# Kernel optimization log

Measured on AMD Instinct MI355X. Metric: run time of the kernel, lower is better.

Reference implementation:

```python
import jax, jax.numpy as jnp
import numpy as np

N_HEADS = 16
HEAD_DIM = 64
HIDDEN = 1024
LN_EPS = 1e-6

def setup_inputs() -> dict:
    key = jax.random.key(0)
    ks = jax.random.split(key, 8)
    B, L, H = 2, 2048, HIDDEN
    s = 1.0 / np.sqrt(H)
    return {
        "q": jax.random.normal(ks[0], (B, L, H), jnp.float32),
        "k": jax.random.normal(ks[1], (B, L, H), jnp.float32),
        "v": jax.random.normal(ks[2], (B, L, H), jnp.float32),
        "w_qs": jax.random.normal(ks[3], (H, N_HEADS * HEAD_DIM), jnp.float32) * s,
        "w_ks": jax.random.normal(ks[4], (H, N_HEADS * HEAD_DIM), jnp.float32) * s,
        "w_vs": jax.random.normal(ks[5], (H, N_HEADS * HEAD_DIM), jnp.float32) * s,
        "w_fc": jax.random.normal(ks[6], (N_HEADS * HEAD_DIM, H), jnp.float32) * s,
        "ln_gamma": jnp.ones((H,), jnp.float32),
        "ln_beta": jnp.zeros((H,), jnp.float32),
    }

def reference(q, k, v, w_qs, w_ks, w_vs, w_fc, ln_gamma, ln_beta):
    B, Lq, H = q.shape
    residual = q
    # projections -> [B, heads, L, head_dim]
    qh = (q @ w_qs).reshape(B, Lq, N_HEADS, HEAD_DIM).transpose(0, 2, 1, 3)
    kh = (k @ w_ks).reshape(B, -1, N_HEADS, HEAD_DIM).transpose(0, 2, 1, 3)
    vh = (v @ w_vs).reshape(B, -1, N_HEADS, HEAD_DIM).transpose(0, 2, 1, 3)
    temp = jnp.asarray(HEAD_DIM ** 0.5, qh.dtype)
    scores = jnp.einsum("bhqd,bhkd->bhqk", qh / temp, kh)  # [B,H,Lq,Lk]
    attn = jax.nn.softmax(scores, axis=-1)  # dropout = identity (eval)
    out = jnp.einsum("bhqk,bhkd->bhqd", attn, vh)
    out = out.transpose(0, 2, 1, 3).reshape(B, Lq, N_HEADS * HEAD_DIM)
    out = out @ w_fc  # dropout = identity (eval)
    x = residual + out
    mu = jnp.mean(x, axis=-1, keepdims=True)
    var = jnp.var(x, axis=-1, keepdims=True)
    y = (x - mu) * jax.lax.rsqrt(var + LN_EPS) * ln_gamma + ln_beta
    return (y, attn)
```

## Files before the change

kernel.cpp:

```cpp
#include <hip/hip_runtime.h>
#include <stdint.h>

#define NHEADS 16
#define HDIM   64
#define HID    1024
#define SEQ    2048
#define NB     2

typedef short s16x8 __attribute__((ext_vector_type(8)));
typedef float f32x4 __attribute__((ext_vector_type(4)));

__device__ __forceinline__ short f2bf(float f) {
  union { float f; unsigned u; } x; x.f = f;
  unsigned r = (x.u + 0x7FFFu + ((x.u >> 16) & 1u)) >> 16;
  return (short)r;
}

__device__ __forceinline__ void gload16(const void* g, void* l) {
  __builtin_amdgcn_global_load_lds(
      (const __attribute__((address_space(1))) unsigned int*)g,
      (__attribute__((address_space(3))) unsigned int*)l, 16, 0, 0);
}

__global__ __launch_bounds__(256)
void prep(const float* __restrict__ w0, const float* __restrict__ w1,
          const float* __restrict__ w2, const float* __restrict__ w3,
          const float* __restrict__ q, const float* __restrict__ k,
          const float* __restrict__ v,
          unsigned short* __restrict__ d0, unsigned short* __restrict__ d1,
          unsigned short* __restrict__ d2, unsigned short* __restrict__ d3,
          unsigned short* __restrict__ qb, unsigned short* __restrict__ kb,
          unsigned short* __restrict__ vb)
{
  const int z = blockIdx.z;
  if (z < 4) {
    const float* src = z == 0 ? w0 : z == 1 ? w1 : z == 2 ? w2 : w3;
    unsigned short* dst = z == 0 ? d0 : z == 1 ? d1 : z == 2 ? d2 : d3;
    __shared__ float t[32][33];
    const int tx = threadIdx.x & 31, ty = threadIdx.x >> 5;
    const int x0 = (blockIdx.x & 31) * 32, y0 = (blockIdx.x >> 5) * 32;
#pragma unroll
    for (int i = 0; i < 4; ++i) {
      const int r = ty + i * 8;
      t[r][tx] = src[(size_t)(y0 + r) * HID + (x0 + tx)];
    }
    __syncthreads();
#pragma unroll
    for (int i = 0; i < 4; ++i) {
      const int r = ty + i * 8;
      dst[(size_t)(x0 + r) * HID + (y0 + tx)] = (unsigned short)f2bf(t[tx][r]);
    }
  } else {
    const float* s = z == 4 ? q : z == 5 ? k : v;
    unsigned short* d = z == 4 ? qb : z == 5 ? kb : vb;
#pragma unroll
    for (int c = 0; c < 2; ++c) {
      const size_t i = (size_t)blockIdx.x * 4096 + c * 2048 + threadIdx.x * 8;
      const float4 f0 = ((const float4*)(s + i))[0];
      const float4 f1 = ((const float4*)(s + i))[1];
      s16x8 o;
      o[0] = f2bf(f0.x); o[1] = f2bf(f0.y); o[2] = f2bf(f0.z); o[3] = f2bf(f0.w);
      o[4] = f2bf(f1.x); o[5] = f2bf(f1.y); o[6] = f2bf(f1.z); o[7] = f2bf(f1.w);
      *(s16x8*)(d + i) = o;
    }
  }
}

__global__ __launch_bounds__(256, 3)
void proj_gemm(const unsigned short* __restrict__ qb, const unsigned short* __restrict__ kb,
               const unsigned short* __restrict__ vb,
               const unsigned short* __restrict__ wqt, const unsigned short* __restrict__ wkt,
               const unsigned short* __restrict__ wvt,
               unsigned short* __restrict__ Qh, unsigned short* __restrict__ Kh,
               unsigned short* __restrict__ Vt)
{
  __shared__ unsigned short As[128 * 64];
  __shared__ unsigned short Bs[128 * 64];
  const int tid = threadIdx.x, lane = tid & 63, w = tid >> 6;
  const int lg = lane >> 4, ll = lane & 15;
  const int wm = w & 1, wn = w >> 1;
  const int z = blockIdx.z;
  const int m0 = blockIdx.x * 128, n0 = blockIdx.y * 128;
  const int xorv = (ll & 7) << 4;

  const unsigned short* A  = z == 0 ? qb : z == 1 ? kb : vb;
  const unsigned short* Bt = z == 0 ? wqt : z == 1 ? wkt : wvt;
  const float alpha = z == 0 ? 0.125f : 1.0f;

  f32x4 acc[4][4];
#pragma unroll
  for (int m = 0; m < 4; ++m)
#pragma unroll
    for (int n = 0; n < 4; ++n) acc[m][n] = (f32x4)0.f;

  int rS[4], cbS[4];
#pragma unroll
  for (int c = 0; c < 4; ++c) {
    const int b = (w * 4 + c) * 1024 + lane * 16;
    rS[c] = b >> 7;
    cbS[c] = (b & 127) ^ ((rS[c] & 7) << 4);
  }

  for (int k0 = 0; k0 < HID; k0 += 64) {
    __syncthreads();
#pragma unroll
    for (int c = 0; c < 4; ++c) {
      gload16((const char*)A + ((((size_t)(m0 + rS[c]) * HID + k0) << 1) + cbS[c]),
              (char*)As + (w * 4 + c) * 1024);
      gload16((const char*)Bt + ((((size_t)(n0 + rS[c]) * HID + k0) << 1) + cbS[c]),
              (char*)Bs + (w * 4 + c) * 1024);
    }
    __syncthreads();
#pragma unroll
    for (int kk = 0; kk < 2; ++kk) {
      const int cb2 = kk * 64 + lg * 16;
      s16x8 a[4], b[4];
#pragma unroll
      for (int m = 0; m < 4; ++m)
        a[m] = *(const s16x8*)((const char*)As + ((((wm * 64 + m * 16 + ll) << 7) + cb2) ^ xorv));
#pragma unroll
      for (int n = 0; n < 4; ++n)
        b[n] = *(const s16x8*)((const char*)Bs + ((((wn * 64 + n * 16 + ll) << 7) + cb2) ^ xorv));
#pragma unroll
      for (int m = 0; m < 4; ++m)
#pragma unroll
        for (int n = 0; n < 4; ++n)
          acc[m][n] = __builtin_amdgcn_mfma_f32_16x16x32_bf16(a[m], b[n], acc[m][n], 0, 0, 0);
    }
  }

#pragma unroll
  for (int m = 0; m < 4; ++m)
#pragma unroll
    for (int n = 0; n < 4; ++n)
#pragma unroll
      for (int r = 0; r < 4; ++r) {
        const int row = m0 + wm * 64 + m * 16 + lg * 4 + r;
        const int col = n0 + wn * 64 + n * 16 + ll;
        const int bb = row >> 11, l = row & (SEQ - 1);
        const int h = col >> 6, d = col & (HDIM - 1);
        const unsigned short o = (unsigned short)f2bf(acc[m][n][r] * alpha);
        if (z < 2) {
          unsigned short* out = z == 0 ? Qh : Kh;
          out[(((size_t)(bb * NHEADS + h) * SEQ + l) * HDIM) + d] = o;
        } else {
          Vt[(((size_t)(bb * NHEADS + h) * HDIM + d) * SEQ) + l] = o;
        }
      }
}

__global__ __launch_bounds__(256, 4)
void fc_gemm(const unsigned short* __restrict__ A, const unsigned short* __restrict__ Bt,
             float* __restrict__ C, const float* __restrict__ resid)
{
  __shared__ unsigned short As[64 * 64];
  __shared__ unsigned short Bs[128 * 64];
  const int tid = threadIdx.x, lane = tid & 63, w = tid >> 6;
  const int lg = lane >> 4, ll = lane & 15;
  const int wm = w & 1, wn = w >> 1;
  const int m0 = blockIdx.x * 64, n0 = blockIdx.y * 128;
  const int xorv = (ll & 7) << 4;

  f32x4 acc[2][4];
#pragma unroll
  for (int m = 0; m < 2; ++m)
#pragma unroll
    for (int n = 0; n < 4; ++n) acc[m][n] = (f32x4)0.f;

  int rA[2], cA[2], rB[4], cB[4];
#pragma unroll
  for (int c = 0; c < 2; ++c) {
    const int b = (w * 2 + c) * 1024 + lane * 16;
    rA[c] = b >> 7; cA[c] = (b & 127) ^ ((rA[c] & 7) << 4);
  }
#pragma unroll
  for (int c = 0; c < 4; ++c) {
    const int b = (w * 4 + c) * 1024 + lane * 16;
    rB[c] = b >> 7; cB[c] = (b & 127) ^ ((rB[c] & 7) << 4);
  }

  for (int k0 = 0; k0 < HID; k0 += 64) {
    __syncthreads();
#pragma unroll
    for (int c = 0; c < 2; ++c)
      gload16((const char*)A + ((((size_t)(m0 + rA[c]) * HID + k0) << 1) + cA[c]),
              (char*)As + (w * 2 + c) * 1024);
#pragma unroll
    for (int c = 0; c < 4; ++c)
      gload16((const char*)Bt + ((((size_t)(n0 + rB[c]) * HID + k0) << 1) + cB[c]),
              (char*)Bs + (w * 4 + c) * 1024);
    __syncthreads();
#pragma unroll
    for (int kk = 0; kk < 2; ++kk) {
      const int cb2 = kk * 64 + lg * 16;
      s16x8 a[2], b[4];
#pragma unroll
      for (int m = 0; m < 2; ++m)
        a[m] = *(const s16x8*)((const char*)As + ((((wm * 32 + m * 16 + ll) << 7) + cb2) ^ xorv));
#pragma unroll
      for (int n = 0; n < 4; ++n)
        b[n] = *(const s16x8*)((const char*)Bs + ((((wn * 64 + n * 16 + ll) << 7) + cb2) ^ xorv));
#pragma unroll
      for (int m = 0; m < 2; ++m)
#pragma unroll
        for (int n = 0; n < 4; ++n)
          acc[m][n] = __builtin_amdgcn_mfma_f32_16x16x32_bf16(a[m], b[n], acc[m][n], 0, 0, 0);
    }
  }

#pragma unroll
  for (int m = 0; m < 2; ++m)
#pragma unroll
    for (int n = 0; n < 4; ++n)
#pragma unroll
      for (int r = 0; r < 4; ++r) {
        const int row = m0 + wm * 32 + m * 16 + lg * 4 + r;
        const int col = n0 + wn * 64 + n * 16 + ll;
        const size_t idx = (size_t)row * HID + col;
        C[idx] = acc[m][n][r] + resid[idx];
      }
}

__global__ __launch_bounds__(256, 3)
void fused_attn(const unsigned short* __restrict__ Qh,
                const unsigned short* __restrict__ Kh,
                const unsigned short* __restrict__ Vt,
                float* __restrict__ attn,
                unsigned short* __restrict__ Ofc)
{
  __shared__ unsigned short BufA[128 * 64];
  __shared__ unsigned short BufB[128 * 64];
  __shared__ unsigned short Ps[128][72];
  const int tid = threadIdx.x, lane = tid & 63, w = tid >> 6;
  const int lg = lane >> 4, ll = lane & 15;
  const int xorv = (ll & 7) << 4;

  const int lin = blockIdx.y * gridDim.x + blockIdx.x;
  const int lin2 = (lin & 7) * 64 + (lin >> 3);
  const int z = lin2 >> 4, qb = lin2 & 15;
  const int bb = z >> 4, h = z & 15;
  const int m0 = qb * 128;

  const unsigned short* Qz = Qh + (size_t)z * SEQ * HDIM;
  const unsigned short* Kz = Kh + (size_t)z * SEQ * HDIM;
  const unsigned short* Vz = Vt + (size_t)z * HDIM * SEQ;
  float* Az = attn + (size_t)z * SEQ * SEQ;

  int rK[4], cbK[4], rV[4], cbV[4];
#pragma unroll
  for (int c = 0; c < 4; ++c) {
    const int b = (w * 4 + c) * 1024 + lane * 16;
    rK[c] = b >> 7; cbK[c] = (b & 127) ^ ((rK[c] & 7) << 4);
    rV[c] = b >> 8; cbV[c] = (b & 255) ^ ((rV[c] & 7) << 4);
  }

  s16x8 qf[2][2];
#pragma unroll
  for (int m = 0; m < 2; ++m)
#pragma unroll
    for (int kk = 0; kk < 2; ++kk)
      qf[m][kk] = *(const s16x8*)(Qz + (size_t)(m0 + w * 32 + m * 16 + ll) * HDIM
                                  + kk * 32 + lg * 8);

  float sml[8];
#pragma unroll
  for (int i = 0; i < 8; ++i) sml[i] = 0.f;

#pragma unroll
  for (int c = 0; c < 4; ++c)
    gload16((const char*)Kz + ((((size_t)(0 * 128 + rK[c]) * HDIM) << 1) + cbK[c]),
            (char*)BufA + (w * 4 + c) * 1024);
  __syncthreads();
  for (int j = 0; j < 16; ++j) {
    char* cur = (char*)((j & 1) ? BufB : BufA);
    char* nxt = (char*)((j & 1) ? BufA : BufB);
    if (j < 15) {
#pragma unroll
      for (int c = 0; c < 4; ++c)
        gload16((const char*)Kz + ((((size_t)((j + 1) * 128 + rK[c]) * HDIM) << 1) + cbK[c]),
                nxt + (w * 4 + c) * 1024);
    }
    f32x4 s[2][8];
#pragma unroll
    for (int m = 0; m < 2; ++m)
#pragma unroll
      for (int n = 0; n < 8; ++n) s[m][n] = (f32x4)0.f;
#pragma unroll
    for (int kk = 0; kk < 2; ++kk) {
      const int cb2 = kk * 64 + lg * 16;
      s16x8 bk[8];
#pragma unroll
      for (int n = 0; n < 8; ++n)
        bk[n] = *(const s16x8*)(cur + ((((n * 16 + ll) << 7) + cb2) ^ xorv));
#pragma unroll
      for (int m = 0; m < 2; ++m)
#pragma unroll
        for (int n = 0; n < 8; ++n)
          s[m][n] = __builtin_amdgcn_mfma_f32_16x16x32_bf16(qf[m][kk], bk[n], s[m][n], 0, 0, 0);
    }
#pragma unroll
    for (int m = 0; m < 2; ++m)
#pragma unroll
      for (int r = 0; r < 4; ++r) {
        const int i = m * 4 + r;
#pragma unroll
        for (int n = 0; n < 8; ++n) sml[i] += __expf(s[m][n][r]);
      }
    __syncthreads();
  }
  float inv[8];
#pragma unroll
  for (int i = 0; i < 8; ++i) {
    float su = sml[i];
#pragma unroll
    for (int off = 1; off < 16; off <<= 1) su += __shfl_xor(su, off, 64);
    inv[i] = 1.0f / su;
  }

  f32x4 ao[2][4];
#pragma unroll
  for (int m = 0; m < 2; ++m)
#pragma unroll
    for (int n = 0; n < 4; ++n) ao[m][n] = (f32x4)0.f;

  for (int j = 0; j < 16; ++j) {
    __syncthreads();
#pragma unroll
    for (int c = 0; c < 4; ++c) {
      gload16((const char*)Kz + ((((size_t)(j * 128 + rK[c]) * HDIM) << 1) + cbK[c]),
              (char*)BufA + (w * 4 + c) * 1024);
      gload16((const char*)Vz + ((((size_t)rV[c] * SEQ + j * 128) << 1) + cbV[c]),
              (char*)BufB + (w * 4 + c) * 1024);
    }
    __syncthreads();
    f32x4 s[2][8];
#pragma unroll
    for (int m = 0; m < 2; ++m)
#pragma unroll
      for (int n = 0; n < 8; ++n) s[m][n] = (f32x4)0.f;
#pragma unroll
    for (int kk = 0; kk < 2; ++kk) {
      const int cb2 = kk * 64 + lg * 16;
      s16x8 bk[8];
#pragma unroll
      for (int n = 0; n < 8; ++n)
        bk[n] = *(const s16x8*)((const char*)BufA + ((((n * 16 + ll) << 7) + cb2) ^ xorv));
#pragma unroll
      for (int m = 0; m < 2; ++m)
#pragma unroll
        for (int n = 0; n < 8; ++n)
          s[m][n] = __builtin_amdgcn_mfma_f32_16x16x32_bf16(qf[m][kk], bk[n], s[m][n], 0, 0, 0);
    }
#pragma unroll
    for (int h2 = 0; h2 < 2; ++h2) {
#pragma unroll
      for (int m = 0; m < 2; ++m)
#pragma unroll
        for (int r = 0; r < 4; ++r) {
          const int i = m * 4 + r;
          const int rowl = w * 32 + m * 16 + lg * 4 + r;
          float* dst = Az + (size_t)(m0 + rowl) * SEQ + j * 128 + h2 * 64 + ll;
#pragma unroll
          for (int nn = 0; nn < 4; ++nn) {
            const float p = __expf(s[m][h2 * 4 + nn][r]) * inv[i];
            __builtin_nontemporal_store(p, dst + nn * 16);
            Ps[rowl][nn * 16 + ll] = (unsigned short)f2bf(p);
          }
        }
#pragma unroll
      for (int kkl = 0; kkl < 2; ++kkl) {
        const int cb2v = (h2 * 2 + kkl) * 64 + lg * 16;
        s16x8 pa[2], vbf[4];
#pragma unroll
        for (int m = 0; m < 2; ++m)
          pa[m] = *(const s16x8*)&Ps[w * 32 + m * 16 + ll][kkl * 32 + lg * 8];
#pragma unroll
        for (int n = 0; n < 4; ++n)
          vbf[n] = *(const s16x8*)((const char*)BufB + ((((n * 16 + ll) << 8) + cb2v) ^ xorv));
#pragma unroll
        for (int m = 0; m < 2; ++m)
#pragma unroll
          for (int n = 0; n < 4; ++n)
            ao[m][n] = __builtin_amdgcn_mfma_f32_16x16x32_bf16(pa[m], vbf[n], ao[m][n], 0, 0, 0);
      }
    }
  }

#pragma unroll
  for (int m = 0; m < 2; ++m)
#pragma unroll
    for (int n = 0; n < 4; ++n)
#pragma unroll
      for (int r = 0; r < 4; ++r) {
        const int qrow = m0 + w * 32 + m * 16 + lg * 4 + r;
        const int d = n * 16 + ll;
        Ofc[((size_t)bb * SEQ + qrow) * HID + h * HDIM + d] =
            (unsigned short)f2bf(ao[m][n][r]);
      }
}

__global__ __launch_bounds__(256)
void ln_kernel(const float* __restrict__ x, const float* __restrict__ gamma,
               const float* __restrict__ beta, float* __restrict__ y)
{
  const int tid = threadIdx.x;
  const size_t row = blockIdx.x;
  const float4 v = ((const float4*)(x + row * HID))[tid];
  float s = v.x + v.y + v.z + v.w;
  float q = v.x * v.x + v.y * v.y + v.z * v.z + v.w * v.w;
#pragma unroll
  for (int off = 32; off; off >>= 1) {
    s += __shfl_xor(s, off, 64);
    q += __shfl_xor(q, off, 64);
  }
  __shared__ float ps[4], pq[4];
  const int wid = tid >> 6, lane = tid & 63;
  if (lane == 0) { ps[wid] = s; pq[wid] = q; }
  __syncthreads();
  const float ts = ps[0] + ps[1] + ps[2] + ps[3];
  const float tq = pq[0] + pq[1] + pq[2] + pq[3];
  const float mu = ts * (1.0f / HID);
  const float var = tq * (1.0f / HID) - mu * mu;
  const float rs = rsqrtf(var + 1e-6f);
  const float4 g = ((const float4*)gamma)[tid];
  const float4 bb = ((const float4*)beta)[tid];
  float4 o;
  o.x = (v.x - mu) * rs * g.x + bb.x;
  o.y = (v.y - mu) * rs * g.y + bb.y;
  o.z = (v.z - mu) * rs * g.z + bb.z;
  o.w = (v.w - mu) * rs * g.w + bb.w;
  ((float4*)(y + row * HID))[tid] = o;
}

extern "C" void kernel_launch(void* const* d_in, const int* in_sizes, int n_in,
                              void* d_out, int out_size, void* d_ws, size_t ws_size,
                              hipStream_t stream)
{
  (void)in_sizes; (void)n_in; (void)out_size; (void)ws_size;
  const float* q     = (const float*)d_in[0];
  const float* k     = (const float*)d_in[1];
  const float* v     = (const float*)d_in[2];
  const float* w_qs  = (const float*)d_in[3];
  const float* w_ks  = (const float*)d_in[4];
  const float* w_vs  = (const float*)d_in[5];
  const float* w_fc  = (const float*)d_in[6];
  const float* gamma = (const float*)d_in[7];
  const float* beta  = (const float*)d_in[8];

  char* ws = (char*)d_ws;
  unsigned short* wqt = (unsigned short*)(ws);
  unsigned short* wkt = (unsigned short*)(ws + ((size_t)2 << 20));
  unsigned short* wvt = (unsigned short*)(ws + ((size_t)4 << 20));
  unsigned short* wft = (unsigned short*)(ws + ((size_t)6 << 20));
  unsigned short* qb  = (unsigned short*)(ws + ((size_t)8 << 20));
  unsigned short* kb  = (unsigned short*)(ws + ((size_t)16 << 20));
  unsigned short* vb  = (unsigned short*)(ws + ((size_t)24 << 20));
  unsigned short* Qh  = (unsigned short*)(ws + ((size_t)32 << 20));
  unsigned short* Kh  = (unsigned short*)(ws + ((size_t)40 << 20));
  unsigned short* Vt  = (unsigned short*)(ws + ((size_t)48 << 20));
  unsigned short* Ofc = qb;
  float*          xres = (float*)(ws + ((size_t)16 << 20));

  float* y_out = (float*)d_out;
  float* attn  = (float*)d_out + (size_t)NB * SEQ * HID;

  const dim3 b256(256, 1, 1);

  prep<<<dim3(1024, 1, 7), b256, 0, stream>>>(
      w_qs, w_ks, w_vs, w_fc, q, k, v, wqt, wkt, wvt, wft, qb, kb, vb);

  proj_gemm<<<dim3(32, 8, 3), b256, 0, stream>>>(qb, kb, vb, wqt, wkt, wvt, Qh, Kh, Vt);

  fused_attn<<<dim3(16, 32, 1), b256, 0, stream>>>(Qh, Kh, Vt, attn, Ofc);

  fc_gemm<<<dim3(64, 8, 1), b256, 0, stream>>>(Ofc, wft, xres, q);

  ln_kernel<<<dim3(NB * SEQ, 1, 1), b256, 0, stream>>>(xres, gamma, beta, y_out);
}
```

Baseline: 246.5 us.

## Double-buffer K/V loads in attention second pass with 64-key tiles

The second attention pass previously loaded a 128-key K tile and V tile into shared memory synchronously each iteration, with two barriers. It now uses 64-key tiles, double-buffered, prefetching the next K/V tiles with async global-to-LDS loads while computing the current one, and keeps one barrier per iteration. Shared memory is merged into one base array so the buffers can be split differently across the two passes. The cost is twice as many iterations and barriers, plus a smaller per-iteration work granule.

```diff
diff --git a/kernel.cpp b/kernel.cpp
--- a/kernel.cpp
+++ b/kernel.cpp
@@ -228,9 +228,8 @@
                 float* __restrict__ attn,
                 unsigned short* __restrict__ Ofc)
 {
-  __shared__ unsigned short BufA[128 * 64];
-  __shared__ unsigned short BufB[128 * 64];
-  __shared__ unsigned short Ps[128][72];
+  __shared__ char sbase[32 * 1024 + 128 * 72 * 2];
+  unsigned short (*Ps)[72] = (unsigned short (*)[72])(sbase + 32 * 1024);
   const int tid = threadIdx.x, lane = tid & 63, w = tid >> 6;
   const int lg = lane >> 4, ll = lane & 15;
   const int xorv = (ll & 7) << 4;
@@ -246,12 +245,17 @@
   const unsigned short* Vz = Vt + (size_t)z * HDIM * SEQ;
   float* Az = attn + (size_t)z * SEQ * SEQ;
 
-  int rK[4], cbK[4], rV[4], cbV[4];
+  int rK[4], cbK[4];
 #pragma unroll
   for (int c = 0; c < 4; ++c) {
     const int b = (w * 4 + c) * 1024 + lane * 16;
     rK[c] = b >> 7; cbK[c] = (b & 127) ^ ((rK[c] & 7) << 4);
-    rV[c] = b >> 8; cbV[c] = (b & 255) ^ ((rV[c] & 7) << 4);
+  }
+  int r2[2], cb2s[2];
+#pragma unroll
+  for (int c = 0; c < 2; ++c) {
+    const int b = (w * 2 + c) * 1024 + lane * 16;
+    r2[c] = b >> 7; cb2s[c] = (b & 127) ^ ((r2[c] & 7) << 4);
   }
 
   s16x8 qf[2][2];
@@ -268,12 +272,12 @@
 
 #pragma unroll
   for (int c = 0; c < 4; ++c)
-    gload16((const char*)Kz + ((((size_t)(0 * 128 + rK[c]) * HDIM) << 1) + cbK[c]),
-            (char*)BufA + (w * 4 + c) * 1024);
+    gload16((const char*)Kz + ((((size_t)rK[c] * HDIM) << 1) + cbK[c]),
+            sbase + (w * 4 + c) * 1024);
   __syncthreads();
   for (int j = 0; j < 16; ++j) {
-    char* cur = (char*)((j & 1) ? BufB : BufA);
-    char* nxt = (char*)((j & 1) ? BufA : BufB);
+    char* cur = sbase + (j & 1) * 16384;
+    char* nxt = sbase + ((j & 1) ^ 1) * 16384;
     if (j < 15) {
 #pragma unroll
       for (int c = 0; c < 4; ++c)
@@ -323,67 +327,77 @@
 #pragma unroll
     for (int n = 0; n < 4; ++n) ao[m][n] = (f32x4)0.f;
 
-  for (int j = 0; j < 16; ++j) {
-    __syncthreads();
-#pragma unroll
-    for (int c = 0; c < 4; ++c) {
-      gload16((const char*)Kz + ((((size_t)(j * 128 + rK[c]) * HDIM) << 1) + cbK[c]),
-              (char*)BufA + (w * 4 + c) * 1024);
-      gload16((const char*)Vz + ((((size_t)rV[c] * SEQ + j * 128) << 1) + cbV[c]),
-              (char*)BufB + (w * 4 + c) * 1024);
-    }
-    __syncthreads();
-    f32x4 s[2][8];
+#pragma unroll
+  for (int c = 0; c < 2; ++c) {
+    gload16((const char*)Kz + ((((size_t)r2[c] * HDIM) << 1) + cb2s[c]),
+            sbase + (w * 2 + c) * 1024);
+    gload16((const char*)Vz + ((((size_t)r2[c] * SEQ) << 1) + cb2s[c]),
+            sbase + 16384 + (w * 2 + c) * 1024);
+  }
+  __syncthreads();
+  for (int j = 0; j < 32; ++j) {
+    char* curK = sbase + (j & 1) * 8192;
+    char* curV = sbase + 16384 + (j & 1) * 8192;
+    char* nxtK = sbase + ((j & 1) ^ 1) * 8192;
+    char* nxtV = sbase + 16384 + ((j & 1) ^ 1) * 8192;
+    if (j < 31) {
+#pragma unroll
+      for (int c = 0; c < 2; ++c) {
+        gload16((const char*)Kz + ((((size_t)((j + 1) * 64 + r2[c]) * HDIM) << 1) + cb2s[c]),
+                nxtK + (w * 2 + c) * 1024);
+        gload16((const char*)Vz + ((((size_t)(r2[c] * SEQ + (j + 1) * 64)) << 1) + cb2s[c]),
+                nxtV + (w * 2 + c) * 1024);
+      }
+    }
+    f32x4 s[2][4];
 #pragma unroll
     for (int m = 0; m < 2; ++m)
 #pragma unroll
-      for (int n = 0; n < 8; ++n) s[m][n] = (f32x4)0.f;
+      for (int n = 0; n < 4; ++n) s[m][n] = (f32x4)0.f;
 #pragma unroll
     for (int kk = 0; kk < 2; ++kk) {
       const int cb2 = kk * 64 + lg * 16;
-      s16x8 bk[8];
-#pragma unroll
-      for (int n = 0; n < 8; ++n)
-        bk[n] = *(const s16x8*)((const char*)BufA + ((((n * 16 + ll) << 7) + cb2) ^ xorv));
-#pragma unroll
-      for (int m = 0; m < 2; ++m)
-#pragma unroll
-        for (int n = 0; n < 8; ++n)
+      s16x8 bk[4];
+#pragma unroll
+      for (int n = 0; n < 4; ++n)
+        bk[n] = *(const s16x8*)(curK + ((((n * 16 + ll) << 7) + cb2) ^ xorv));
+#pragma unroll
+      for (int m = 0; m < 2; ++m)
+#pragma unroll
+        for (int n = 0; n < 4; ++n)
           s[m][n] = __builtin_amdgcn_mfma_f32_16x16x32_bf16(qf[m][kk], bk[n], s[m][n], 0, 0, 0);
     }
 #pragma unroll
-    for (int h2 = 0; h2 < 2; ++h2) {
-#pragma unroll
-      for (int m = 0; m < 2; ++m)
-#pragma unroll
-        for (int r = 0; r < 4; ++r) {
-          const int i = m * 4 + r;
-          const int rowl = w * 32 + m * 16 + lg * 4 + r;
-          float* dst = Az + (size_t)(m0 + rowl) * SEQ + j * 128 + h2 * 64 + ll;
-#pragma unroll
-          for (int nn = 0; nn < 4; ++nn) {
-            const float p = __expf(s[m][h2 * 4 + nn][r]) * inv[i];
-            __builtin_nontemporal_store(p, dst + nn * 16);
-            Ps[rowl][nn * 16 + ll] = (unsigned short)f2bf(p);
-          }
+    for (int m = 0; m < 2; ++m)
+#pragma unroll
+      for (int r = 0; r < 4; ++r) {
+        const int i = m * 4 + r;
+        const int rowl = w * 32 + m * 16 + lg * 4 + r;
+        float* dst = Az + (size_t)(m0 + rowl) * SEQ + j * 64 + ll;
+#pragma unroll
+        for (int nn = 0; nn < 4; ++nn) {
+          const float p = __expf(s[m][nn][r]) * inv[i];
+          __builtin_nontemporal_store(p, dst + nn * 16);
+          Ps[rowl][nn * 16 + ll] = (unsigned short)f2bf(p);
         }
-#pragma unroll
-      for (int kkl = 0; kkl < 2; ++kkl) {
-        const int cb2v = (h2 * 2 + kkl) * 64 + lg * 16;
-        s16x8 pa[2], vbf[4];
-#pragma unroll
-        for (int m = 0; m < 2; ++m)
-          pa[m] = *(const s16x8*)&Ps[w * 32 + m * 16 + ll][kkl * 32 + lg * 8];
+      }
+#pragma unroll
+    for (int kkl = 0; kkl < 2; ++kkl) {
+      const int cbv = kkl * 64 + lg * 16;
+      s16x8 pa[2], vbf[4];
+#pragma unroll
+      for (int m = 0; m < 2; ++m)
+        pa[m] = *(const s16x8*)&Ps[w * 32 + m * 16 + ll][kkl * 32 + lg * 8];
+#pragma unroll
+      for (int n = 0; n < 4; ++n)
+        vbf[n] = *(const s16x8*)(curV + ((((n * 16 + ll) << 7) + cbv) ^ xorv));
+#pragma unroll
+      for (int m = 0; m < 2; ++m)
 #pragma unroll
         for (int n = 0; n < 4; ++n)
-          vbf[n] = *(const s16x8*)((const char*)BufB + ((((n * 16 + ll) << 8) + cb2v) ^ xorv));
-#pragma unroll
-        for (int m = 0; m < 2; ++m)
-#pragma unroll
-          for (int n = 0; n < 4; ++n)
-            ao[m][n] = __builtin_amdgcn_mfma_f32_16x16x32_bf16(pa[m], vbf[n], ao[m][n], 0, 0, 0);
-      }
-    }
+          ao[m][n] = __builtin_amdgcn_mfma_f32_16x16x32_bf16(pa[m], vbf[n], ao[m][n], 0, 0, 0);
+    }
+    __syncthreads();
   }
 
 #pragma unroll
```

Measured after the change: 275.7 us. +11.8%, slower.
